# Optimization experiments

Measured on AMD Instinct MI355X. Metric: run time of the kernel, lower is better.

## Reference

```python
import jax, jax.numpy as jnp
import numpy as np
from jax import lax

WINDOW_SIZE = 11
SIGMA = 1.5
DATA_RANGE = 1.0
C1 = (0.01 * DATA_RANGE) ** 2
C2 = (0.03 * DATA_RANGE) ** 2


def _gaussian_window(channels: int) -> jnp.ndarray:
    coords = jnp.arange(WINDOW_SIZE, dtype=jnp.float32) - (WINDOW_SIZE // 2)
    g = jnp.exp(-coords ** 2 / (2.0 * SIGMA ** 2))
    g = g / g.sum()
    k2d = jnp.outer(g, g)  # [K, K]
    # depthwise kernel [C, 1, K, K] (OIHW with feature_group_count=C)
    return jnp.broadcast_to(k2d[None, None], (channels, 1, WINDOW_SIZE, WINDOW_SIZE))


def _depthwise_conv(x: jnp.ndarray, window: jnp.ndarray) -> jnp.ndarray:
    pad = WINDOW_SIZE // 2
    return lax.conv_general_dilated(
        x, window,
        window_strides=(1, 1),
        padding=[(pad, pad), (pad, pad)],
        dimension_numbers=("NCHW", "OIHW", "NCHW"),
        feature_group_count=x.shape[1],
    )


def setup_inputs() -> dict:
    key = jax.random.key(0)
    k1, k2 = jax.random.split(key)
    shape = (16, 3, 512, 512)
    pred = jax.random.uniform(k1, shape, dtype=jnp.float32)
    target = jax.random.uniform(k2, shape, dtype=jnp.float32)
    return {"pred": pred, "target": target}


def reference(pred, target):
    channels = pred.shape[1]
    window = _gaussian_window(channels)

    mu1 = _depthwise_conv(pred, window)
    mu2 = _depthwise_conv(target, window)
    mu1_sq = mu1 ** 2
    mu2_sq = mu2 ** 2
    mu1_mu2 = mu1 * mu2

    sigma1_sq = _depthwise_conv(pred * pred, window) - mu1_sq
    sigma2_sq = _depthwise_conv(target * target, window) - mu2_sq
    sigma12 = _depthwise_conv(pred * target, window) - mu1_mu2

    ssim_map = ((2.0 * mu1_mu2 + C1) * (2.0 * sigma12 + C2)) / (
        (mu1_sq + mu2_sq + C1) * (sigma1_sq + sigma2_sq + C2)
    )
    return 1.0 - ssim_map.mean()
```

## Files before the change

### kernel.cpp

```cpp
#include <hip/hip_runtime.h>
#include <cmath>

#define HH 512
#define WW 512
#define TW 32
#define TH 32
#define INH 42
#define TWP 33
#define NTHREADS 256
#define NXT 16
#define NYT 16
#define NBLK (NXT * NYT * 48)
#define C1F 0.0001f
#define C2F 0.0009f

struct GaussW { float w[11]; };

__global__ __launch_bounds__(NTHREADS) void ssim_tile_kernel(
    const float* __restrict__ pred, const float* __restrict__ targ,
    float* __restrict__ partial, GaussW gw)
{
    __shared__ __align__(16) float hp[INH][TWP][4];
    __shared__ float wred[4];

    const int tid = threadIdx.x;

    const int lid = (blockIdx.z * gridDim.y + blockIdx.y) * gridDim.x + blockIdx.x;
    const int wi  = (lid & 7) * (NBLK / 8) + (lid >> 3);
    const int bx  = wi & (NXT - 1);
    const int by  = (wi >> 4) & (NYT - 1);
    const int bz  = wi >> 8;

    const int gx0 = bx * TW;
    const int gy0 = by * TH - 5;
    const size_t plane = (size_t)bz * (size_t)(HH * WW);

    const bool xinterior = (bx > 0) && (bx < NXT - 1);

    if (xinterior) {
        for (int i = tid; i < INH * 8; i += NTHREADS) {
            int r = i >> 3;
            int g = i & 7;
            int c0 = g << 2;
            int gr = gy0 + r;
            float p[16], t[16];
            if ((unsigned)gr < (unsigned)HH) {
                const float* prow = pred + plane + (size_t)gr * WW + (gx0 + c0 - 6);
                const float* trow = targ + plane + (size_t)gr * WW + (gx0 + c0 - 6);
                *(float2*)&p[0]  = *(const float2*)(prow);
                *(float4*)&p[2]  = *(const float4*)(prow + 2);
                *(float4*)&p[6]  = *(const float4*)(prow + 6);
                *(float4*)&p[10] = *(const float4*)(prow + 10);
                *(float2*)&p[14] = *(const float2*)(prow + 14);
                *(float2*)&t[0]  = *(const float2*)(trow);
                *(float4*)&t[2]  = *(const float4*)(trow + 2);
                *(float4*)&t[6]  = *(const float4*)(trow + 6);
                *(float4*)&t[10] = *(const float4*)(trow + 10);
                *(float2*)&t[14] = *(const float2*)(trow + 14);
            } else {
                #pragma unroll
                for (int m = 0; m < 16; m++) { p[m] = 0.f; t[m] = 0.f; }
            }

            #pragma unroll
            for (int m = 1; m < 15; m++) {
                float pv = p[m], tv = t[m];
                p[m] = pv + tv;
                t[m] = pv - tv;
            }

            float sa[4]  = {0,0,0,0}, sb[4]  = {0,0,0,0};
            float saa[4] = {0,0,0,0}, sbb[4] = {0,0,0,0};
            #pragma unroll
            for (int k = 0; k < 11; k++) {
                float wk = gw.w[k];
                #pragma unroll
                for (int o = 0; o < 4; o++) {
                    float av = p[o + k + 1], bv = t[o + k + 1];
                    float wa = wk * av, wb = wk * bv;
                    sa[o]  += wa;
                    sb[o]  += wb;
                    saa[o] += wa * av;
                    sbb[o] += wb * bv;
                }
            }
            #pragma unroll
            for (int o = 0; o < 4; o++) {
                int phys = (g ^ (o << 1)) + (o << 3);
                *(float4*)&hp[r][phys][0] = make_float4(sa[o], sb[o], saa[o], sbb[o]);
            }
        }
    } else {
        for (int i = tid; i < INH * 8; i += NTHREADS) {
            int r = i >> 3;
            int g = i & 7;
            int c0 = g << 2;
            int gr = gy0 + r;
            float p[14], t[14];
            if ((unsigned)gr < (unsigned)HH) {
                const size_t rb = plane + (size_t)gr * WW;
                int cbase = gx0 + c0 - 5;
                #pragma unroll
                for (int m = 0; m < 14; m++) {
                    int gc = cbase + m;
                    int cc = min(max(gc, 0), WW - 1);
                    bool in = (unsigned)gc < (unsigned)WW;
                    float pv = pred[rb + cc];
                    float tv = targ[rb + cc];
                    p[m] = in ? pv : 0.f;
                    t[m] = in ? tv : 0.f;
                }
            } else {
                #pragma unroll
                for (int m = 0; m < 14; m++) { p[m] = 0.f; t[m] = 0.f; }
            }

            #pragma unroll
            for (int m = 0; m < 14; m++) {
                float pv = p[m], tv = t[m];
                p[m] = pv + tv;
                t[m] = pv - tv;
            }

            float sa[4]  = {0,0,0,0}, sb[4]  = {0,0,0,0};
            float saa[4] = {0,0,0,0}, sbb[4] = {0,0,0,0};
            #pragma unroll
            for (int k = 0; k < 11; k++) {
                float wk = gw.w[k];
                #pragma unroll
                for (int o = 0; o < 4; o++) {
                    float av = p[o + k], bv = t[o + k];
                    float wa = wk * av, wb = wk * bv;
                    sa[o]  += wa;
                    sb[o]  += wb;
                    saa[o] += wa * av;
                    sbb[o] += wb * bv;
                }
            }
            #pragma unroll
            for (int o = 0; o < 4; o++) {
                int phys = (g ^ (o << 1)) + (o << 3);
                *(float4*)&hp[r][phys][0] = make_float4(sa[o], sb[o], saa[o], sbb[o]);
            }
        }
    }
    __syncthreads();

    float local = 0.f;
    {
        const int c0 = tid & 31;
        const int r0 = (tid >> 5) << 2;
        const int pc = ((c0 >> 2) ^ ((c0 & 3) << 1)) + ((c0 & 3) << 3);
        const float* hbase = &hp[r0][pc][0];

        float4 acc[4];
        #pragma unroll
        for (int rr = 0; rr < 4; rr++)
            acc[rr] = make_float4(0.f, 0.f, 0.f, 0.f);

        #pragma unroll
        for (int jj = 0; jj < 14; jj++) {
            float4 v = *(const float4*)(hbase + (size_t)jj * (TWP * 4));
            #pragma unroll
            for (int rr = 0; rr < 4; rr++) {
                int k = jj - rr;
                if (k >= 0 && k < 11) {
                    float wk = gw.w[k];
                    acc[rr].x += wk * v.x;
                    acc[rr].y += wk * v.y;
                    acc[rr].z += wk * v.z;
                    acc[rr].w += wk * v.w;
                }
            }
        }

        #pragma unroll
        for (int rr = 0; rr < 4; rr++) {
            float A  = acc[rr].x, Bv = acc[rr].y;
            float EA = acc[rr].z, EB = acc[rr].w;
            float A2 = A * A, B2 = Bv * Bv;
            float S  = 0.5f  * (A2 + B2);
            float P  = 0.25f * (A2 - B2);
            float Ep = 0.5f  * (EA + EB);
            float Ec = 0.25f * (EA - EB);
            float num = (2.f * P + C1F) * (2.f * (Ec - P) + C2F);
            float den = (S + C1F) * ((Ep - S) + C2F);
            local += num * __builtin_amdgcn_rcpf(den);
        }
    }

    #pragma unroll
    for (int off = 32; off > 0; off >>= 1)
        local += __shfl_down(local, off, 64);
    int lane = tid & 63, wid = tid >> 6;
    if (lane == 0) wred[wid] = local;
    __syncthreads();
    if (tid == 0)
        partial[lid] = wred[0] + wred[1] + wred[2] + wred[3];
}

__global__ __launch_bounds__(256) void ssim_finalize_kernel(
    const float* __restrict__ partial, float inv_count,
    float* __restrict__ out)
{
    __shared__ float sm[4];
    float s = 0.f;
    #pragma unroll
    for (int i = 0; i < NBLK / 4 / 256; i++) {
        float4 v = *(const float4*)&partial[(threadIdx.x + i * 256) * 4];
        s += (v.x + v.y) + (v.z + v.w);
    }
    #pragma unroll
    for (int off = 32; off > 0; off >>= 1)
        s += __shfl_down(s, off, 64);
    int lane = threadIdx.x & 63, wid = threadIdx.x >> 6;
    if (lane == 0) sm[wid] = s;
    __syncthreads();
    if (threadIdx.x == 0)
        out[0] = 1.0f - (sm[0] + sm[1] + sm[2] + sm[3]) * inv_count;
}

extern "C" void kernel_launch(void* const* d_in, const int* in_sizes, int n_in,
                              void* d_out, int out_size, void* d_ws, size_t ws_size,
                              hipStream_t stream)
{
    const float* pred = (const float*)d_in[0];
    const float* targ = (const float*)d_in[1];
    float* out = (float*)d_out;
    float* partial = (float*)d_ws;

    const int total = in_sizes[0];
    const int nplanes = total / (HH * WW);

    GaussW gw;
    double g[11], s = 0.0;
    for (int i = 0; i < 11; i++) {
        double d = (double)(i - 5);
        g[i] = exp(-d * d / 4.5);
        s += g[i];
    }
    for (int i = 0; i < 11; i++) gw.w[i] = (float)(g[i] / s);

    dim3 grid(NXT, NYT, nplanes);
    ssim_tile_kernel<<<grid, NTHREADS, 0, stream>>>(pred, targ, partial, gw);

    const float inv_count = 1.0f / (float)total;
    ssim_finalize_kernel<<<1, 256, 0, stream>>>(partial, inv_count, out);
}
```

Baseline: 154.4 us.

## Use taller 64-row tiles with 512 threads and vectorized edge-block loads

Doubles the tile height to 64 rows with 512 threads per block, cutting the vertical halo overhead from 42/32 to 74/64 rows of horizontal-pass work and loads. It also replaces the scalar clamped edge-column path with aligned float4 loads plus register shifts, and unifies the interior and edge branches. The cost is a larger shared-memory tile and fewer blocks, which may lower occupancy. The plane count is now hardcoded to 48.

```diff
diff --git a/kernel.cpp b/kernel.cpp
--- a/kernel.cpp
+++ b/kernel.cpp
@@ -4,24 +4,39 @@
 #define HH 512
 #define WW 512
 #define TW 32
-#define TH 32
-#define INH 42
+#define TH 64
+#define INH 74
 #define TWP 33
-#define NTHREADS 256
+#define NTHREADS 512
 #define NXT 16
-#define NYT 16
-#define NBLK (NXT * NYT * 48)
+#define NYT 8
+#define NPL 48
+#define NBLK (NXT * NYT * NPL)
 #define C1F 0.0001f
 #define C2F 0.0009f
 
 struct GaussW { float w[11]; };
+
+__device__ __forceinline__ void load16a4(const float* __restrict__ p, float v[16]) {
+    *(float4*)&v[0]  = *(const float4*)(p);
+    *(float4*)&v[4]  = *(const float4*)(p + 4);
+    *(float4*)&v[8]  = *(const float4*)(p + 8);
+    *(float4*)&v[12] = *(const float4*)(p + 12);
+}
+__device__ __forceinline__ void load16a2(const float* __restrict__ p, float v[16]) {
+    *(float2*)&v[0]  = *(const float2*)(p);
+    *(float4*)&v[2]  = *(const float4*)(p + 2);
+    *(float4*)&v[6]  = *(const float4*)(p + 6);
+    *(float4*)&v[10] = *(const float4*)(p + 10);
+    *(float2*)&v[14] = *(const float2*)(p + 14);
+}
 
 __global__ __launch_bounds__(NTHREADS) void ssim_tile_kernel(
     const float* __restrict__ pred, const float* __restrict__ targ,
     float* __restrict__ partial, GaussW gw)
 {
     __shared__ __align__(16) float hp[INH][TWP][4];
-    __shared__ float wred[4];
+    __shared__ float wred[8];
 
     const int tid = threadIdx.x;
 
@@ -29,119 +44,103 @@
     const int wi  = (lid & 7) * (NBLK / 8) + (lid >> 3);
     const int bx  = wi & (NXT - 1);
     const int by  = (wi >> 4) & (NYT - 1);
-    const int bz  = wi >> 8;
+    const int bz  = wi >> 7;
 
     const int gx0 = bx * TW;
     const int gy0 = by * TH - 5;
     const size_t plane = (size_t)bz * (size_t)(HH * WW);
 
-    const bool xinterior = (bx > 0) && (bx < NXT - 1);
-
-    if (xinterior) {
-        for (int i = tid; i < INH * 8; i += NTHREADS) {
-            int r = i >> 3;
-            int g = i & 7;
-            int c0 = g << 2;
-            int gr = gy0 + r;
-            float p[16], t[16];
-            if ((unsigned)gr < (unsigned)HH) {
-                const float* prow = pred + plane + (size_t)gr * WW + (gx0 + c0 - 6);
-                const float* trow = targ + plane + (size_t)gr * WW + (gx0 + c0 - 6);
-                *(float2*)&p[0]  = *(const float2*)(prow);
-                *(float4*)&p[2]  = *(const float4*)(prow + 2);
-                *(float4*)&p[6]  = *(const float4*)(prow + 6);
-                *(float4*)&p[10] = *(const float4*)(prow + 10);
-                *(float2*)&p[14] = *(const float2*)(prow + 14);
-                *(float2*)&t[0]  = *(const float2*)(trow);
-                *(float4*)&t[2]  = *(const float4*)(trow + 2);
-                *(float4*)&t[6]  = *(const float4*)(trow + 6);
-                *(float4*)&t[10] = *(const float4*)(trow + 10);
-                *(float2*)&t[14] = *(const float2*)(trow + 14);
-            } else {
-                #pragma unroll
-                for (int m = 0; m < 16; m++) { p[m] = 0.f; t[m] = 0.f; }
-            }
-
-            #pragma unroll
-            for (int m = 1; m < 15; m++) {
-                float pv = p[m], tv = t[m];
-                p[m] = pv + tv;
-                t[m] = pv - tv;
-            }
-
-            float sa[4]  = {0,0,0,0}, sb[4]  = {0,0,0,0};
-            float saa[4] = {0,0,0,0}, sbb[4] = {0,0,0,0};
-            #pragma unroll
-            for (int k = 0; k < 11; k++) {
-                float wk = gw.w[k];
-                #pragma unroll
-                for (int o = 0; o < 4; o++) {
-                    float av = p[o + k + 1], bv = t[o + k + 1];
-                    float wa = wk * av, wb = wk * bv;
-                    sa[o]  += wa;
-                    sb[o]  += wb;
-                    saa[o] += wa * av;
-                    sbb[o] += wb * bv;
-                }
-            }
+    const bool lblk = (bx == 0);
+    const bool rblk = (bx == NXT - 1);
+
+    for (int i = tid; i < INH * 8; i += NTHREADS) {
+        int r = i >> 3;
+        int g = i & 7;
+        int c0 = g << 2;
+        int gr = gy0 + r;
+
+        if ((unsigned)gr >= (unsigned)HH) {
+            float4 z = make_float4(0.f, 0.f, 0.f, 0.f);
             #pragma unroll
             for (int o = 0; o < 4; o++) {
                 int phys = (g ^ (o << 1)) + (o << 3);
-                *(float4*)&hp[r][phys][0] = make_float4(sa[o], sb[o], saa[o], sbb[o]);
-            }
-        }
-    } else {
-        for (int i = tid; i < INH * 8; i += NTHREADS) {
-            int r = i >> 3;
-            int g = i & 7;
-            int c0 = g << 2;
-            int gr = gy0 + r;
-            float p[14], t[14];
-            if ((unsigned)gr < (unsigned)HH) {
-                const size_t rb = plane + (size_t)gr * WW;
-                int cbase = gx0 + c0 - 5;
-                #pragma unroll
-                for (int m = 0; m < 14; m++) {
-                    int gc = cbase + m;
-                    int cc = min(max(gc, 0), WW - 1);
-                    bool in = (unsigned)gc < (unsigned)WW;
-                    float pv = pred[rb + cc];
-                    float tv = targ[rb + cc];
-                    p[m] = in ? pv : 0.f;
-                    t[m] = in ? tv : 0.f;
+                *(float4*)&hp[r][phys][0] = z;
+            }
+            continue;
+        }
+
+        const float* prow = pred + plane + (size_t)gr * WW;
+        const float* trow = targ + plane + (size_t)gr * WW;
+
+        float a[14], b[14];
+        if (lblk && g < 2) {
+            float P[16], T[16];
+            load16a4(prow, P);
+            load16a4(trow, T);
+            if (g == 0) {
+                #pragma unroll
+                for (int j = 0; j < 14; j++) {
+                    float pv = (j >= 5) ? P[j - 5] : 0.f;
+                    float tv = (j >= 5) ? T[j - 5] : 0.f;
+                    a[j] = pv + tv; b[j] = pv - tv;
                 }
             } else {
                 #pragma unroll
-                for (int m = 0; m < 14; m++) { p[m] = 0.f; t[m] = 0.f; }
-            }
-
-            #pragma unroll
-            for (int m = 0; m < 14; m++) {
-                float pv = p[m], tv = t[m];
-                p[m] = pv + tv;
-                t[m] = pv - tv;
-            }
-
-            float sa[4]  = {0,0,0,0}, sb[4]  = {0,0,0,0};
-            float saa[4] = {0,0,0,0}, sbb[4] = {0,0,0,0};
-            #pragma unroll
-            for (int k = 0; k < 11; k++) {
-                float wk = gw.w[k];
-                #pragma unroll
-                for (int o = 0; o < 4; o++) {
-                    float av = p[o + k], bv = t[o + k];
-                    float wa = wk * av, wb = wk * bv;
-                    sa[o]  += wa;
-                    sb[o]  += wb;
-                    saa[o] += wa * av;
-                    sbb[o] += wb * bv;
-                }
-            }
+                for (int j = 0; j < 14; j++) {
+                    float pv = (j >= 1) ? P[j - 1] : 0.f;
+                    float tv = (j >= 1) ? T[j - 1] : 0.f;
+                    a[j] = pv + tv; b[j] = pv - tv;
+                }
+            }
+        } else if (rblk && g > 5) {
+            float P[16], T[16];
+            load16a4(prow + (WW - 16), P);
+            load16a4(trow + (WW - 16), T);
+            if (g == 6) {
+                #pragma unroll
+                for (int j = 0; j < 14; j++) {
+                    float pv = (j <= 12) ? P[j + 3] : 0.f;
+                    float tv = (j <= 12) ? T[j + 3] : 0.f;
+                    a[j] = pv + tv; b[j] = pv - tv;
+                }
+            } else {
+                #pragma unroll
+                for (int j = 0; j < 14; j++) {
+                    float pv = (j <= 8) ? P[j + 7] : 0.f;
+                    float tv = (j <= 8) ? T[j + 7] : 0.f;
+                    a[j] = pv + tv; b[j] = pv - tv;
+                }
+            }
+        } else {
+            float P[16], T[16];
+            load16a2(prow + gx0 + c0 - 6, P);
+            load16a2(trow + gx0 + c0 - 6, T);
+            #pragma unroll
+            for (int j = 0; j < 14; j++) {
+                float pv = P[j + 1], tv = T[j + 1];
+                a[j] = pv + tv; b[j] = pv - tv;
+            }
+        }
+
+        float sa[4]  = {0,0,0,0}, sb[4]  = {0,0,0,0};
+        float saa[4] = {0,0,0,0}, sbb[4] = {0,0,0,0};
+        #pragma unroll
+        for (int k = 0; k < 11; k++) {
+            float wk = gw.w[k];
             #pragma unroll
             for (int o = 0; o < 4; o++) {
-                int phys = (g ^ (o << 1)) + (o << 3);
-                *(float4*)&hp[r][phys][0] = make_float4(sa[o], sb[o], saa[o], sbb[o]);
-            }
+                float av = a[o + k], bv = b[o + k];
+                float wa = wk * av, wb = wk * bv;
+                sa[o]  += wa;
+                sb[o]  += wb;
+                saa[o] += wa * av;
+                sbb[o] += wb * bv;
+            }
+        }
+        #pragma unroll
+        for (int o = 0; o < 4; o++) {
+            int phys = (g ^ (o << 1)) + (o << 3);
+            *(float4*)&hp[r][phys][0] = make_float4(sa[o], sb[o], saa[o], sbb[o]);
         }
     }
     __syncthreads();
@@ -195,8 +194,12 @@
     int lane = tid & 63, wid = tid >> 6;
     if (lane == 0) wred[wid] = local;
     __syncthreads();
-    if (tid == 0)
-        partial[lid] = wred[0] + wred[1] + wred[2] + wred[3];
+    if (tid == 0) {
+        float s = 0.f;
+        #pragma unroll
+        for (int w2 = 0; w2 < 8; w2++) s += wred[w2];
+        partial[lid] = s;
+    }
 }
 
 __global__ __launch_bounds__(256) void ssim_finalize_kernel(
@@ -230,7 +233,6 @@
     float* partial = (float*)d_ws;
 
     const int total = in_sizes[0];
-    const int nplanes = total / (HH * WW);
 
     GaussW gw;
     double g[11], s = 0.0;
@@ -241,7 +243,7 @@
     }
     for (int i = 0; i < 11; i++) gw.w[i] = (float)(g[i] / s);
 
-    dim3 grid(NXT, NYT, nplanes);
+    dim3 grid(NXT, NYT, NPL);
     ssim_tile_kernel<<<grid, NTHREADS, 0, stream>>>(pred, targ, partial, gw);
 
     const float inv_count = 1.0f / (float)total;
```

Result: faster. 147.5 us (-4.5%).
